# Optimization experiments

Measured on AMD Instinct MI355X. Metric: run time of the kernel, lower is better.

Reference implementation:

```python
import jax, jax.numpy as jnp
import numpy as np

# Dims: B nodes, C channels (num_features), X = irrep_out.dim, Y = U basis size, correlation = 3
B, C, X, Y = 128, 128, 3, 16


def setup_inputs() -> dict:
    key = jax.random.key(0)
    k1, k2 = jax.random.split(key)
    # x: [B, C, X, Y, Y, Y]  (spare dims 'wxv' = X, Y, Y ; trailing 'i' = Y)
    x = jax.random.normal(k1, (B, C, X, Y, Y, Y), dtype=jnp.float32)
    # node_attributes: [B, C, Y]
    node_attributes = jax.random.normal(k2, (B, C, Y), dtype=jnp.float32)
    return {"x": x, "node_attributes": node_attributes}


def reference(x, node_attributes):
    # Faithful to instruction 'bcwxvi,bci->bcwxv' (spare = SPARE[:3] = 'wxv')
    # Contracts only the last axis i; output [B, C, X, Y, Y].
    return jnp.einsum('bcwxvi,bci->bcwxv', x, node_attributes)
```

## Files before the change

### kernel.cpp

```cpp
#include <hip/hip_runtime.h>


constexpr int ROWS_PER_BC = 3 * 16 * 16;
constexpr int YN = 16;

__global__ __launch_bounds__(256) void feat_contract_kernel(
    const float* __restrict__ x,
    const float* __restrict__ na,
    float* __restrict__ out) {
    const int bc = blockIdx.y;
    const int t  = threadIdx.x;
    const int q  = t & 3;
    const int lr = t >> 2;
    const int row_in_slice = blockIdx.x * 64 + lr;

    const float4 aq = *reinterpret_cast<const float4*>(na + (size_t)bc * YN + q * 4);

    const size_t row = (size_t)bc * ROWS_PER_BC + row_in_slice;
    const float4 xq = *reinterpret_cast<const float4*>(x + row * YN + q * 4);

    float s = xq.x * aq.x + xq.y * aq.y + xq.z * aq.z + xq.w * aq.w;

    s += __shfl_xor(s, 1, 64);
    s += __shfl_xor(s, 2, 64);

    if (q == 0) {
        out[row] = s;
    }
}

extern "C" void kernel_launch(void* const* d_in, const int* in_sizes, int n_in,
                              void* d_out, int out_size, void* d_ws, size_t ws_size,
                              hipStream_t stream) {
    const float* x  = (const float*)d_in[0];
    const float* na = (const float*)d_in[1];
    float* out = (float*)d_out;

    const int BC = in_sizes[1] / YN;
    dim3 grid(ROWS_PER_BC / 64, BC);
    dim3 block(256);
    feat_contract_kernel<<<grid, block, 0, stream>>>(x, na, out);
}
```

Baseline: 984.1 us.

## Process one whole (b,c) slice per block with batched float4 loads

Each block now handles an entire (b,c) slice, 768 rows, instead of 64 rows. Every thread issues 12 independent float4 loads up front and then reduces each row with shuffles. This cuts the grid from about 196K blocks to 16K and raises per-thread memory-level parallelism, so each block reads the node-attribute vector once. In exchange, register use per thread rises and there are fewer waves in flight, which could reduce occupancy.

Result: slower. 1.016 ms (+3.2%).

```diff
diff --git a/kernel.cpp b/kernel.cpp
--- a/kernel.cpp
+++ b/kernel.cpp
@@ -1,43 +1,49 @@
 #include <hip/hip_runtime.h>
 
 
-constexpr int ROWS_PER_BC = 3 * 16 * 16;
-constexpr int YN = 16;
+constexpr int YN          = 16;
+constexpr int ROWS_PER_BC = 3 * YN * YN;
+constexpr int F4_PER_BC   = ROWS_PER_BC * 4;
+constexpr int THREADS     = 256;
+constexpr int ITERS       = F4_PER_BC / THREADS;
 
-__global__ __launch_bounds__(256) void feat_contract_kernel(
-    const float* __restrict__ x,
-    const float* __restrict__ na,
+__global__ __launch_bounds__(THREADS) void feat_contract_kernel(
+    const float4* __restrict__ x4,
+    const float*  __restrict__ na,
     float* __restrict__ out) {
-    const int bc = blockIdx.y;
+    const int bc = blockIdx.x;
     const int t  = threadIdx.x;
     const int q  = t & 3;
-    const int lr = t >> 2;
-    const int row_in_slice = blockIdx.x * 64 + lr;
 
     const float4 aq = *reinterpret_cast<const float4*>(na + (size_t)bc * YN + q * 4);
 
-    const size_t row = (size_t)bc * ROWS_PER_BC + row_in_slice;
-    const float4 xq = *reinterpret_cast<const float4*>(x + row * YN + q * 4);
+    const float4* xb = x4 + (size_t)bc * F4_PER_BC + t;
+    float* ob = out + (size_t)bc * ROWS_PER_BC + (t >> 2);
 
-    float s = xq.x * aq.x + xq.y * aq.y + xq.z * aq.z + xq.w * aq.w;
+    float4 v[ITERS];
+#pragma unroll
+    for (int i = 0; i < ITERS; ++i) v[i] = xb[i * THREADS];
 
-    s += __shfl_xor(s, 1, 64);
-    s += __shfl_xor(s, 2, 64);
-
-    if (q == 0) {
-        out[row] = s;
+#pragma unroll
+    for (int i = 0; i < ITERS; ++i) {
+        float s = v[i].x * aq.x + v[i].y * aq.y + v[i].z * aq.z + v[i].w * aq.w;
+        s += __shfl_xor(s, 1, 64);
+        s += __shfl_xor(s, 2, 64);
+        if (q == 0) {
+            ob[i * 64] = s;
+        }
     }
 }
 
 extern "C" void kernel_launch(void* const* d_in, const int* in_sizes, int n_in,
                               void* d_out, int out_size, void* d_ws, size_t ws_size,
                               hipStream_t stream) {
-    const float* x  = (const float*)d_in[0];
-    const float* na = (const float*)d_in[1];
+    const float4* x4 = (const float4*)d_in[0];
+    const float*  na = (const float*)d_in[1];
     float* out = (float*)d_out;
 
     const int BC = in_sizes[1] / YN;
-    dim3 grid(ROWS_PER_BC / 64, BC);
-    dim3 block(256);
-    feat_contract_kernel<<<grid, block, 0, stream>>>(x, na, out);
+    dim3 grid(BC);
+    dim3 block(THREADS);
+    feat_contract_kernel<<<grid, block, 0, stream>>>(x4, na, out);
 }
```
